# Optimization experiments

Hardware: AMD Instinct MI355X
Metric: run time of the kernel (lower is better)

## Reference

```python
import jax, jax.numpy as jnp
import numpy as np

N = 100000   # n_nodes
C = 128      # n_map
S = 6        # num_scales
E = 200000   # edges per pre/suc scale
EL = 50000   # left/right edges
L = 4        # fusion layers
EPS = 1e-5


def _gn(x, w, b):
    # GroupNorm(num_groups=1) on (N, C): normalize over channel dim per row.
    m = jnp.mean(x, axis=-1, keepdims=True)
    v = jnp.mean((x - m) ** 2, axis=-1, keepdims=True)
    return (x - m) * jax.lax.rsqrt(v + EPS) * w + b


def setup_inputs() -> dict:
    key = jax.random.key(0)
    ks = jax.random.split(key, 24)
    sc = 1.0 / np.sqrt(C)
    inp = {
        "feat": jax.random.normal(ks[0], (N, C), jnp.float32),
        "pre_u": jax.random.randint(ks[1], (S, E), 0, N, jnp.int32),
        "pre_v": jax.random.randint(ks[2], (S, E), 0, N, jnp.int32),
        "suc_u": jax.random.randint(ks[3], (S, E), 0, N, jnp.int32),
        "suc_v": jax.random.randint(ks[4], (S, E), 0, N, jnp.int32),
        "left_u": jax.random.randint(ks[5], (EL,), 0, N, jnp.int32),
        "left_v": jax.random.randint(ks[6], (EL,), 0, N, jnp.int32),
        "right_u": jax.random.randint(ks[7], (EL,), 0, N, jnp.int32),
        "right_v": jax.random.randint(ks[8], (EL,), 0, N, jnp.int32),
        # learned params, stacked over the 4 fusion layers
        "W_ctr": jax.random.normal(ks[9], (L, C, C), jnp.float32) * sc,
        "norm_w": jnp.ones((L, C), jnp.float32),
        "norm_b": jnp.zeros((L, C), jnp.float32),
        "W_ctr2": jax.random.normal(ks[10], (L, C, C), jnp.float32) * sc,
        "ctr2_w": jnp.ones((L, C), jnp.float32),
        "ctr2_b": jnp.zeros((L, C), jnp.float32),
        "W_left": jax.random.normal(ks[11], (L, C, C), jnp.float32) * sc,
        "W_right": jax.random.normal(ks[12], (L, C, C), jnp.float32) * sc,
        "W_pre": jax.random.normal(ks[13], (L, S, C, C), jnp.float32) * sc,
        "W_suc": jax.random.normal(ks[14], (L, S, C, C), jnp.float32) * sc,
    }
    return inp


def reference(feat, pre_u, pre_v, suc_u, suc_v, left_u, left_v, right_u, right_v,
              W_ctr, norm_w, norm_b, W_ctr2, ctr2_w, ctr2_b,
              W_left, W_right, W_pre, W_suc):
    res = feat
    for i in range(L):
        # ctr linear (bias=False): y = x @ W.T
        temp = feat @ W_ctr[i].T
        # pre/suc multi-scale gather -> per-scale linear -> scatter-add
        msg_pre = jnp.einsum('sef,sgf->seg', feat[pre_v], W_pre[i])  # (S,E,C)
        temp = temp.at[pre_u.reshape(-1)].add(msg_pre.reshape(-1, C))
        msg_suc = jnp.einsum('sef,sgf->seg', feat[suc_v], W_suc[i])
        temp = temp.at[suc_u.reshape(-1)].add(msg_suc.reshape(-1, C))
        # left/right neighbor edges
        temp = temp.at[left_u].add(feat[left_v] @ W_left[i].T)
        temp = temp.at[right_u].add(feat[right_v] @ W_right[i].T)
        # norm -> relu -> ctr2 (linear + GN, no act) -> residual -> relu
        feat = jax.nn.relu(_gn(temp, norm_w[i], norm_b[i]))
        feat = _gn(feat @ W_ctr2[i].T, ctr2_w[i], ctr2_b[i])
        feat = jax.nn.relu(feat + res)
        res = feat
    return feat
```

## Files before the change

### kernel.cpp

```cpp
#include <hip/hip_runtime.h>
#include <hip/hip_bf16.h>

#define NN 100000
#define C 128
#define S 6
#define EE 200000
#define ELR 50000
#define NLAYER 4
#define GN_EPS 1e-5f
#define NBKT 14
#define KCAT (NBKT*C)
#define TOTE (2*S*EE + 2*ELR)
#define MCNT (NBKT*NN)
#define NSCB ((MCNT + 255)/256)
#define NBLK2 ((NN + 127)/128)
#define VMASK 131071

typedef _Float16 f16;
typedef __attribute__((ext_vector_type(4))) _Float16 f16x4;
typedef __attribute__((ext_vector_type(8))) _Float16 f16x8;
typedef __attribute__((ext_vector_type(4))) float f32x4;
typedef __attribute__((ext_vector_type(8))) unsigned short us8;
struct alignas(8) h4 { f16 v[4]; };

__global__ void k_diag(float* out, float mb) { out[0] = mb; }

__global__ void k_wconv(const float* __restrict__ Wpre, const float* __restrict__ Wsuc,
                        const float* __restrict__ Wleft, const float* __restrict__ Wright,
                        const float* __restrict__ Wctr, const float* __restrict__ Wctr2,
                        f16* __restrict__ out) {
  int i = blockIdx.x * blockDim.x + threadIdx.x;
  if (i >= NLAYER * 16 * C * C) return;
  int within = i & (C * C - 1);
  int b = (i >> 14) & 15;
  int layer = i >> 18;
  const float* src;
  if (b < 6)        src = Wpre  + (size_t)(layer * S + b) * C * C;
  else if (b < 12)  src = Wsuc  + (size_t)(layer * S + (b - 6)) * C * C;
  else if (b == 12) src = Wleft  + (size_t)layer * C * C;
  else if (b == 13) src = Wright + (size_t)layer * C * C;
  else if (b == 14) src = Wctr   + (size_t)layer * C * C;
  else              src = Wctr2  + (size_t)layer * C * C;
  out[i] = (f16)src[within];
}

__global__ void k_f2b(const float* __restrict__ in, f16* __restrict__ out) {
  int i = blockIdx.x * blockDim.x + threadIdx.x;
  if (i >= NN * C / 4) return;
  f32x4 v = *(const f32x4*)(in + (long)i * 4);
  h4 o;
  #pragma unroll
  for (int r = 0; r < 4; r++) o.v[r] = (f16)v[r];
  *(h4*)(out + (long)i * 4) = o;
}

__global__ void k_count(const int* __restrict__ pu, const int* __restrict__ su,
                        const int* __restrict__ lu, const int* __restrict__ ru,
                        int* __restrict__ counts) {
  int i = blockIdx.x * blockDim.x + threadIdx.x;
  if (i >= TOTE) return;
  int u, b;
  if (i < S * EE)                { u = pu[i]; b = i / EE; }
  else if (i < 2 * S * EE)       { int j = i - S * EE; u = su[j]; b = 6 + j / EE; }
  else if (i < 2 * S * EE + ELR) { u = lu[i - 2 * S * EE]; b = 12; }
  else                           { u = ru[i - 2 * S * EE - ELR]; b = 13; }
  atomicAdd(&counts[b * NN + u], 1);
}

__global__ void k_scan1(const int* __restrict__ counts, int* __restrict__ offs, int* __restrict__ bsum) {
  __shared__ int sm[256];
  int t = threadIdx.x;
  int gidx = blockIdx.x * 256 + t;
  int v = (gidx < MCNT) ? counts[gidx] : 0;
  sm[t] = v;
  __syncthreads();
  for (int off = 1; off < 256; off <<= 1) {
    int x = (t >= off) ? sm[t - off] : 0;
    __syncthreads();
    sm[t] += x;
    __syncthreads();
  }
  if (gidx < MCNT) offs[gidx] = sm[t] - v;
  if (t == 255) bsum[blockIdx.x] = sm[255];
}

__global__ void k_scan_mid(int* __restrict__ bsum) {
  __shared__ int sm[1024];
  int t = threadIdx.x;
  int vreg[6];
  int p = 0;
  #pragma unroll
  for (int j = 0; j < 6; j++) {
    int idx = t * 6 + j;
    int x = (idx < NSCB) ? bsum[idx] : 0;
    vreg[j] = x; p += x;
  }
  sm[t] = p;
  __syncthreads();
  for (int off = 1; off < 1024; off <<= 1) {
    int x = (t >= off) ? sm[t - off] : 0;
    __syncthreads();
    sm[t] += x;
    __syncthreads();
  }
  int e = sm[t] - p;
  #pragma unroll
  for (int j = 0; j < 6; j++) {
    int idx = t * 6 + j;
    if (idx < NSCB) { bsum[idx] = e; e += vreg[j]; }
  }
}

__global__ void k_scan3(int* __restrict__ offs, const int* __restrict__ bsum) {
  int gidx = blockIdx.x * 256 + threadIdx.x;
  if (gidx >= MCNT) return;
  offs[gidx] += bsum[gidx >> 8];
}

__global__ void k_fill(const int* __restrict__ pu, const int* __restrict__ pv,
                       const int* __restrict__ su, const int* __restrict__ sv,
                       const int* __restrict__ lu, const int* __restrict__ lv,
                       const int* __restrict__ ru, const int* __restrict__ rv,
                       int* __restrict__ offs, int* __restrict__ col) {
  int i = blockIdx.x * blockDim.x + threadIdx.x;
  if (i >= TOTE) return;
  int u, v, b;
  if (i < S * EE)                { u = pu[i]; v = pv[i]; b = i / EE; }
  else if (i < 2 * S * EE)       { int j = i - S * EE; u = su[j]; v = sv[j]; b = 6 + j / EE; }
  else if (i < 2 * S * EE + ELR) { int j = i - 2 * S * EE; u = lu[j]; v = lv[j]; b = 12; }
  else                           { int j = i - 2 * S * EE - ELR; u = ru[j]; v = rv[j]; b = 13; }
  int pos = atomicAdd(&offs[b * NN + u], 1);
  col[pos] = v;
}

__global__ __launch_bounds__(512) void k_agg(
    const f16* __restrict__ fbf, const int* __restrict__ offs, const int* __restrict__ counts,
    const int* __restrict__ col, f16* __restrict__ Agg, int u0, int nrows) {
  int hw = threadIdx.x >> 5, li = threadIdx.x & 31;
  int cid = blockIdx.x * 16 + hw;
  if (cid >= 14 * nrows) return;
  int ul = cid / 14;
  int b = cid - ul * 14;
  int u = u0 + ul;
  int end = offs[b * NN + u];
  int cnt = counts[b * NN + u];
  int st = end - cnt;
  int cb = li << 2;
  float a0 = 0.f, a1 = 0.f, a2 = 0.f, a3 = 0.f;
  int j = 0;
  for (; j + 1 < cnt; j += 2) {
    int v0 = col[st + j] & VMASK;
    int v1 = col[st + j + 1] & VMASK;
    f16x4 h0 = *(const f16x4*)(fbf + (long)v0 * C + cb);
    f16x4 h1 = *(const f16x4*)(fbf + (long)v1 * C + cb);
    a0 += (float)h0[0] + (float)h1[0];
    a1 += (float)h0[1] + (float)h1[1];
    a2 += (float)h0[2] + (float)h1[2];
    a3 += (float)h0[3] + (float)h1[3];
  }
  if (j < cnt) {
    int v0 = col[st + j] & VMASK;
    f16x4 h0 = *(const f16x4*)(fbf + (long)v0 * C + cb);
    a0 += (float)h0[0]; a1 += (float)h0[1]; a2 += (float)h0[2]; a3 += (float)h0[3];
  }
  h4 o; o.v[0] = (f16)a0; o.v[1] = (f16)a1; o.v[2] = (f16)a2; o.v[3] = (f16)a3;
  *(h4*)(Agg + (long)ul * KCAT + b * C + cb) = o;
}

__global__ __launch_bounds__(256) void k_big(
    const f16* __restrict__ Agg, const f16* __restrict__ fbf, const f16* __restrict__ wb,
    const float* __restrict__ gnw, const float* __restrict__ gnb,
    f16* __restrict__ f1bf, int u0, int nrows) {
  int t = threadIdx.x;
  int wv = t >> 6, lane = t & 63;
  int l15 = lane & 15, g = lane >> 4;
  int row0 = blockIdx.x * 128;

  const f32x4 fz = {0.f, 0.f, 0.f, 0.f};
  f32x4 acc[2][8];
  #pragma unroll
  for (int ri = 0; ri < 2; ri++)
    #pragma unroll
    for (int ci = 0; ci < 8; ci++) acc[ri][ci] = fz;

  const f16x8 hz = {0,0,0,0,0,0,0,0};
  for (int src = 0; src < 15; src++) {
    const f16* wsrc = wb + src * C * C;
    f16x8 Bf[2][4];
    #pragma unroll
    for (int ri = 0; ri < 2; ri++) {
      int r = row0 + wv * 32 + ri * 16 + l15;
      bool ok = (r < nrows);
      #pragma unroll
      for (int kk = 0; kk < 4; kk++) {
        if (ok)
          Bf[ri][kk] = (src < 14)
            ? *(const f16x8*)(Agg + (long)r * KCAT + src * C + kk * 32 + g * 8)
            : *(const f16x8*)(fbf + (long)(u0 + r) * C + kk * 32 + g * 8);
        else Bf[ri][kk] = hz;
      }
    }
    #pragma unroll
    for (int ci = 0; ci < 8; ci++) {
      #pragma unroll
      for (int kk = 0; kk < 4; kk++) {
        f16x8 A = *(const f16x8*)(wsrc + (ci * 16 + l15) * C + kk * 32 + g * 8);
        acc[0][ci] = __builtin_amdgcn_mfma_f32_16x16x32_f16(A, Bf[0][kk], acc[0][ci], 0, 0, 0);
        acc[1][ci] = __builtin_amdgcn_mfma_f32_16x16x32_f16(A, Bf[1][kk], acc[1][ci], 0, 0, 0);
      }
    }
  }

  #pragma unroll
  for (int ri = 0; ri < 2; ri++) {
    float s = 0.f, q = 0.f;
    #pragma unroll
    for (int ci = 0; ci < 8; ci++)
      #pragma unroll
      for (int r2 = 0; r2 < 4; r2++) { float x = acc[ri][ci][r2]; s += x; q += x * x; }
    s += __shfl_xor(s, 16); s += __shfl_xor(s, 32);
    q += __shfl_xor(q, 16); q += __shfl_xor(q, 32);
    float mean = s * (1.0f / C);
    float var = q * (1.0f / C) - mean * mean;
    float inv = rsqrtf(var + GN_EPS);
    int r = row0 + wv * 32 + ri * 16 + l15;
    if (r >= nrows) continue;
    #pragma unroll
    for (int ci = 0; ci < 8; ci++) {
      int ocol = ci * 16 + g * 4;
      h4 o;
      #pragma unroll
      for (int r2 = 0; r2 < 4; r2++) {
        float y = (acc[ri][ci][r2] - mean) * inv * gnw[ocol + r2] + gnb[ocol + r2];
        o.v[r2] = (f16)fmaxf(y, 0.0f);
      }
      *(h4*)(f1bf + (long)(u0 + r) * C + ocol) = o;
    }
  }
}

__global__ __launch_bounds__(256) void k_ctr2(
    const f16* __restrict__ f1bf, const f16* __restrict__ w2,
    f16* __restrict__ fbf, const float* __restrict__ gw, const float* __restrict__ gb,
    float* __restrict__ fout, int last) {
  __shared__ f16 ws[128][136];
  __shared__ float gwb[2][C];
  int t = threadIdx.x;
  int wv = t >> 6, lane = t & 63;
  int l15 = lane & 15, g = lane >> 4;
  int row0 = blockIdx.x * 128;

  if (t < C) gwb[0][t] = gw[t];
  else       gwb[1][t - C] = gb[t - C];
  #pragma unroll
  for (int i = 0; i < 8; i++) {
    int q = t + 256 * i;
    int r = q >> 4, ch = q & 15;
    *(us8*)(&ws[r][ch * 8]) = *(const us8*)(w2 + r * C + ch * 8);
  }

  const f16x8 hz = {0,0,0,0,0,0,0,0};
  f16x8 Bf[2][4];
  #pragma unroll
  for (int ri = 0; ri < 2; ri++) {
    int grow = row0 + wv * 32 + ri * 16 + l15;
    #pragma unroll
    for (int kk = 0; kk < 4; kk++) {
      if (grow < NN)
        Bf[ri][kk] = *(const f16x8*)(f1bf + (long)grow * C + kk * 32 + g * 8);
      else
        Bf[ri][kk] = hz;
    }
  }
  __syncthreads();

  const f32x4 fzero = {0.f, 0.f, 0.f, 0.f};
  f32x4 acc[2][8];
  #pragma unroll
  for (int ri = 0; ri < 2; ri++)
    #pragma unroll
    for (int ci = 0; ci < 8; ci++) acc[ri][ci] = fzero;

  #pragma unroll
  for (int ci = 0; ci < 8; ci++) {
    f16x8 A[4];
    #pragma unroll
    for (int kk = 0; kk < 4; kk++)
      A[kk] = *(const f16x8*)(&ws[ci * 16 + l15][kk * 32 + g * 8]);
    #pragma unroll
    for (int ri = 0; ri < 2; ri++)
      #pragma unroll
      for (int kk = 0; kk < 4; kk++)
        acc[ri][ci] = __builtin_amdgcn_mfma_f32_16x16x32_f16(A[kk], Bf[ri][kk], acc[ri][ci], 0, 0, 0);
  }

  float sv[2], qv[2];
  #pragma unroll
  for (int ri = 0; ri < 2; ri++) {
    float s = 0.f, q = 0.f;
    #pragma unroll
    for (int ci = 0; ci < 8; ci++)
      #pragma unroll
      for (int r = 0; r < 4; r++) { float x = acc[ri][ci][r]; s += x; q += x * x; }
    s += __shfl_xor(s, 16); s += __shfl_xor(s, 32);
    q += __shfl_xor(q, 16); q += __shfl_xor(q, 32);
    sv[ri] = s; qv[ri] = q;
  }

  #pragma unroll
  for (int ri = 0; ri < 2; ri++) {
    float mean = sv[ri] * (1.0f / C);
    float var = qv[ri] * (1.0f / C) - mean * mean;
    float inv = rsqrtf(var + GN_EPS);
    int orow = row0 + wv * 32 + ri * 16 + l15;
    if (orow >= NN) continue;
    #pragma unroll
    for (int ci = 0; ci < 8; ci++) {
      int ocol = ci * 16 + g * 4;
      h4 rr = *(const h4*)(fbf + (long)orow * C + ocol);
      h4 ob;
      f32x4 o;
      #pragma unroll
      for (int r = 0; r < 4; r++) {
        float z = (acc[ri][ci][r] - mean) * inv;
        float y = z * gwb[0][ocol + r] + gwb[1][ocol + r];
        y += (float)rr.v[r];
        y = fmaxf(y, 0.0f);
        o[r] = y;
        ob.v[r] = (f16)y;
      }
      *(h4*)(fbf + (long)orow * C + ocol) = ob;
      if (last) *(f32x4*)(fout + (long)orow * C + ocol) = o;
    }
  }
}

extern "C" void kernel_launch(void* const* d_in, const int* in_sizes, int n_in,
                              void* d_out, int out_size, void* d_ws, size_t ws_size,
                              hipStream_t stream) {
  const float* feat   = (const float*)d_in[0];
  const int* pre_u    = (const int*)d_in[1];
  const int* pre_v    = (const int*)d_in[2];
  const int* suc_u    = (const int*)d_in[3];
  const int* suc_v    = (const int*)d_in[4];
  const int* left_u   = (const int*)d_in[5];
  const int* left_v   = (const int*)d_in[6];
  const int* right_u  = (const int*)d_in[7];
  const int* right_v  = (const int*)d_in[8];
  const float* W_ctr  = (const float*)d_in[9];
  const float* norm_w = (const float*)d_in[10];
  const float* norm_b = (const float*)d_in[11];
  const float* W_ctr2 = (const float*)d_in[12];
  const float* ctr2_w = (const float*)d_in[13];
  const float* ctr2_b = (const float*)d_in[14];
  const float* W_left = (const float*)d_in[15];
  const float* W_right= (const float*)d_in[16];
  const float* W_pre  = (const float*)d_in[17];
  const float* W_suc  = (const float*)d_in[18];
  float* outf = (float*)d_out;

  const size_t NEEDED = 75000000;
  if (ws_size < NEEDED) {
    k_diag<<<1, 1, 0, stream>>>(outf, (float)(ws_size >> 20));
    return;
  }

  char* p = (char*)d_ws;
  auto alloc = [&](size_t bytes) { char* r = p; p += (bytes + 255) & ~(size_t)255; return r; };
  int* col    = (int*)alloc((size_t)TOTE * 4);
  int* counts = (int*)alloc((size_t)MCNT * 4);
  int* offs   = (int*)alloc((size_t)MCNT * 4);
  int* bsum   = (int*)alloc((size_t)8192 * 4);
  f16* wbuf   = (f16*)alloc((size_t)NLAYER * 16 * C * C * 2);
  f16* fbf    = (f16*)alloc((size_t)NN * C * 2);
  f16* f1bf   = (f16*)alloc((size_t)NN * C * 2);

  size_t used = (size_t)(p - (char*)d_ws);
  size_t ws_free = (ws_size > used) ? ws_size - used : 0;
  f16* Agg;
  int CH;
  if (ws_free >= (size_t)NN * KCAT * 2)          { Agg = (f16*)p; CH = NN; }
  else if (ws_free >= (size_t)25000 * KCAT * 2)  { Agg = (f16*)p; CH = 25000; }
  else                                           { Agg = (f16*)d_out; CH = 12500; }

  hipMemsetAsync(counts, 0, (size_t)MCNT * 4, stream);
  k_wconv<<<(NLAYER * 16 * C * C + 255) / 256, 256, 0, stream>>>(W_pre, W_suc, W_left, W_right, W_ctr, W_ctr2, wbuf);
  k_f2b<<<(NN * C / 4 + 255) / 256, 256, 0, stream>>>(feat, fbf);
  k_count<<<(TOTE + 255) / 256, 256, 0, stream>>>(pre_u, suc_u, left_u, right_u, counts);
  k_scan1<<<NSCB, 256, 0, stream>>>(counts, offs, bsum);
  k_scan_mid<<<1, 1024, 0, stream>>>(bsum);
  k_scan3<<<NSCB, 256, 0, stream>>>(offs, bsum);
  k_fill<<<(TOTE + 255) / 256, 256, 0, stream>>>(pre_u, pre_v, suc_u, suc_v,
                                                 left_u, left_v, right_u, right_v, offs, col);

  for (int layer = 0; layer < NLAYER; layer++) {
    const f16* wl = wbuf + (size_t)layer * 16 * C * C;
    for (int u0 = 0; u0 < NN; u0 += CH) {
      int nr = (NN - u0 < CH) ? (NN - u0) : CH;
      int cells = 14 * nr;
      k_agg<<<(cells + 15) / 16, 512, 0, stream>>>(fbf, offs, counts, col, Agg, u0, nr);
      k_big<<<(nr + 127) / 128, 256, 0, stream>>>(Agg, fbf, wl,
                                                  norm_w + (size_t)layer * C, norm_b + (size_t)layer * C,
                                                  f1bf, u0, nr);
    }
    k_ctr2<<<NBLK2, 256, 0, stream>>>(f1bf, wl + 15 * C * C,
                                      fbf, ctr2_w + (size_t)layer * C, ctr2_b + (size_t)layer * C,
                                      outf, layer == NLAYER - 1 ? 1 : 0);
  }
}
```

Baseline: 2.773 ms.

## Fuse ctr2 linear, GroupNorm and residual into the main per-layer GEMM kernel

The big GEMM kernel now stages its normalized ReLU output in LDS with an XOR swizzle, then runs the ctr2 128x128 matmul, GroupNorm, residual add and ReLU in the same block. The next-layer features go to a ping-pong buffer, which removes the separate k_ctr2 launch and the global round trip of the intermediate activation. The B-operand loads are software double-buffered across the 15 source slices so loads overlap the MFMAs. The aggregation buffer is now always chunked at 25000 rows, which adds launches but keeps the Agg working set smaller and possibly more cache-resident. The trade-off is higher register and LDS pressure in the fused kernel, which may lower occupancy.

```diff
diff --git a/kernel.cpp b/kernel.cpp
--- a/kernel.cpp
+++ b/kernel.cpp
@@ -167,48 +167,67 @@
   *(h4*)(Agg + (long)ul * KCAT + b * C + cb) = o;
 }
 
-__global__ __launch_bounds__(256) void k_big(
-    const f16* __restrict__ Agg, const f16* __restrict__ fbf, const f16* __restrict__ wb,
+__global__ __launch_bounds__(256) void k_big2(
+    const f16* __restrict__ Agg, const f16* __restrict__ cur, const f16* __restrict__ wb,
     const float* __restrict__ gnw, const float* __restrict__ gnb,
-    f16* __restrict__ f1bf, int u0, int nrows) {
+    const float* __restrict__ g2w, const float* __restrict__ g2b,
+    f16* __restrict__ nxt, float* __restrict__ fout,
+    int u0, int nrows, int do2, int last) {
+  __shared__ f16 f1s[16384];
   int t = threadIdx.x;
   int wv = t >> 6, lane = t & 63;
   int l15 = lane & 15, g = lane >> 4;
   int row0 = blockIdx.x * 128;
-
-  const f32x4 fz = {0.f, 0.f, 0.f, 0.f};
+  const f16x8 hz = {0,0,0,0,0,0,0,0};
+
   f32x4 acc[2][8];
   #pragma unroll
   for (int ri = 0; ri < 2; ri++)
     #pragma unroll
-    for (int ci = 0; ci < 8; ci++) acc[ri][ci] = fz;
-
-  const f16x8 hz = {0,0,0,0,0,0,0,0};
-  for (int src = 0; src < 15; src++) {
-    const f16* wsrc = wb + src * C * C;
-    f16x8 Bf[2][4];
-    #pragma unroll
-    for (int ri = 0; ri < 2; ri++) {
-      int r = row0 + wv * 32 + ri * 16 + l15;
-      bool ok = (r < nrows);
-      #pragma unroll
-      for (int kk = 0; kk < 4; kk++) {
-        if (ok)
-          Bf[ri][kk] = (src < 14)
-            ? *(const f16x8*)(Agg + (long)r * KCAT + src * C + kk * 32 + g * 8)
-            : *(const f16x8*)(fbf + (long)(u0 + r) * C + kk * 32 + g * 8);
-        else Bf[ri][kk] = hz;
-      }
-    }
-    #pragma unroll
-    for (int ci = 0; ci < 8; ci++) {
-      #pragma unroll
-      for (int kk = 0; kk < 4; kk++) {
-        f16x8 A = *(const f16x8*)(wsrc + (ci * 16 + l15) * C + kk * 32 + g * 8);
-        acc[0][ci] = __builtin_amdgcn_mfma_f32_16x16x32_f16(A, Bf[0][kk], acc[0][ci], 0, 0, 0);
-        acc[1][ci] = __builtin_amdgcn_mfma_f32_16x16x32_f16(A, Bf[1][kk], acc[1][ci], 0, 0, 0);
-      }
-    }
+    for (int ci = 0; ci < 8; ci++) acc[ri][ci] = {0.f, 0.f, 0.f, 0.f};
+
+#define LOADB(SRC, BF)                                                          \
+  {                                                                             \
+    int _s = (SRC);                                                             \
+    _Pragma("unroll")                                                           \
+    for (int ri = 0; ri < 2; ri++) {                                            \
+      int r = row0 + wv * 32 + ri * 16 + l15;                                   \
+      bool ok = (r < nrows);                                                    \
+      _Pragma("unroll")                                                         \
+      for (int kk = 0; kk < 4; kk++) {                                          \
+        if (ok)                                                                 \
+          BF[ri][kk] = (_s < 14)                                                \
+            ? *(const f16x8*)(Agg + (long)r * KCAT + _s * C + kk * 32 + g * 8)  \
+            : *(const f16x8*)(cur + (long)(u0 + r) * C + kk * 32 + g * 8);      \
+        else BF[ri][kk] = hz;                                                   \
+      }                                                                         \
+    }                                                                           \
+  }
+
+#define MFMAS(SRC, BF)                                                          \
+  {                                                                             \
+    const f16* wsrc = wb + (SRC) * C * C;                                       \
+    _Pragma("unroll")                                                           \
+    for (int ci = 0; ci < 8; ci++)                                              \
+      _Pragma("unroll")                                                         \
+      for (int kk = 0; kk < 4; kk++) {                                          \
+        f16x8 A = *(const f16x8*)(wsrc + (ci * 16 + l15) * C + kk * 32 + g * 8);\
+        acc[0][ci] = __builtin_amdgcn_mfma_f32_16x16x32_f16(A, BF[0][kk], acc[0][ci], 0, 0, 0); \
+        acc[1][ci] = __builtin_amdgcn_mfma_f32_16x16x32_f16(A, BF[1][kk], acc[1][ci], 0, 0, 0); \
+      }                                                                         \
+  }
+
+  {
+    f16x8 B0[2][4], B1[2][4];
+    LOADB(0, B0);
+    #pragma unroll
+    for (int sp = 0; sp < 7; sp++) {
+      LOADB(2 * sp + 1, B1);
+      MFMAS(2 * sp, B0);
+      LOADB(2 * sp + 2, B0);
+      MFMAS(2 * sp + 1, B1);
+    }
+    MFMAS(14, B0);
   }
 
   #pragma unroll
@@ -218,6 +237,69 @@
     for (int ci = 0; ci < 8; ci++)
       #pragma unroll
       for (int r2 = 0; r2 < 4; r2++) { float x = acc[ri][ci][r2]; s += x; q += x * x; }
+    s += __shfl_xor(s, 16); s += __shfl_xor(s, 32);
+    q += __shfl_xor(q, 16); q += __shfl_xor(q, 32);
+    float mean = s * (1.0f / C);
+    float var = q * (1.0f / C) - mean * mean;
+    float inv = rsqrtf(var + GN_EPS);
+    int lrow = wv * 32 + ri * 16 + l15;
+    int grow = row0 + lrow;
+    #pragma unroll
+    for (int ci = 0; ci < 8; ci++) {
+      int ocol = ci * 16 + g * 4;
+      h4 o;
+      #pragma unroll
+      for (int r2 = 0; r2 < 4; r2++) {
+        float y = (acc[ri][ci][r2] - mean) * inv * gnw[ocol + r2] + gnb[ocol + r2];
+        o.v[r2] = (f16)fmaxf(y, 0.0f);
+      }
+      if (do2) {
+        int gran = ((ci * 2 + (g >> 1)) ^ (lrow & 7));
+        *(h4*)(&f1s[lrow * 128 + gran * 8 + (g & 1) * 4]) = o;
+      } else if (grow < nrows + u0 - u0 + row0 ? (row0 + lrow) < nrows : false) {
+      }
+      if (!do2 && (row0 + lrow) < nrows)
+        *(h4*)(nxt + (long)(u0 + row0 + lrow) * C + ocol) = o;
+    }
+  }
+  if (!do2) return;
+  __syncthreads();
+
+  f32x4 a2[2][8];
+  #pragma unroll
+  for (int ri = 0; ri < 2; ri++)
+    #pragma unroll
+    for (int ci = 0; ci < 8; ci++) a2[ri][ci] = {0.f, 0.f, 0.f, 0.f};
+
+  {
+    f16x8 B2[2][4];
+    #pragma unroll
+    for (int ri = 0; ri < 2; ri++) {
+      int lrow = wv * 32 + ri * 16 + l15;
+      #pragma unroll
+      for (int kk = 0; kk < 4; kk++) {
+        int gran = (kk * 4 + g) ^ (lrow & 7);
+        B2[ri][kk] = *(const f16x8*)(&f1s[lrow * 128 + gran * 8]);
+      }
+    }
+    const f16* w2 = wb + 15 * C * C;
+    #pragma unroll
+    for (int ci = 0; ci < 8; ci++)
+      #pragma unroll
+      for (int kk = 0; kk < 4; kk++) {
+        f16x8 A = *(const f16x8*)(w2 + (ci * 16 + l15) * C + kk * 32 + g * 8);
+        a2[0][ci] = __builtin_amdgcn_mfma_f32_16x16x32_f16(A, B2[0][kk], a2[0][ci], 0, 0, 0);
+        a2[1][ci] = __builtin_amdgcn_mfma_f32_16x16x32_f16(A, B2[1][kk], a2[1][ci], 0, 0, 0);
+      }
+  }
+
+  #pragma unroll
+  for (int ri = 0; ri < 2; ri++) {
+    float s = 0.f, q = 0.f;
+    #pragma unroll
+    for (int ci = 0; ci < 8; ci++)
+      #pragma unroll
+      for (int r2 = 0; r2 < 4; r2++) { float x = a2[ri][ci][r2]; s += x; q += x * x; }
     s += __shfl_xor(s, 16); s += __shfl_xor(s, 32);
     q += __shfl_xor(q, 16); q += __shfl_xor(q, 32);
     float mean = s * (1.0f / C);
@@ -225,18 +307,28 @@
     float inv = rsqrtf(var + GN_EPS);
     int r = row0 + wv * 32 + ri * 16 + l15;
     if (r >= nrows) continue;
+    long grow = u0 + r;
     #pragma unroll
     for (int ci = 0; ci < 8; ci++) {
       int ocol = ci * 16 + g * 4;
-      h4 o;
+      h4 rr = *(const h4*)(cur + grow * C + ocol);
       #pragma unroll
       for (int r2 = 0; r2 < 4; r2++) {
-        float y = (acc[ri][ci][r2] - mean) * inv * gnw[ocol + r2] + gnb[ocol + r2];
-        o.v[r2] = (f16)fmaxf(y, 0.0f);
-      }
-      *(h4*)(f1bf + (long)(u0 + r) * C + ocol) = o;
-    }
-  }
+        float z = (a2[ri][ci][r2] - mean) * inv;
+        a2[ri][ci][r2] = fmaxf(z * g2w[ocol + r2] + g2b[ocol + r2] + (float)rr.v[r2], 0.0f);
+      }
+      if (last) {
+        *(f32x4*)(fout + grow * C + ocol) = a2[ri][ci];
+      } else {
+        h4 ob;
+        #pragma unroll
+        for (int r2 = 0; r2 < 4; r2++) ob.v[r2] = (f16)a2[ri][ci][r2];
+        *(h4*)(nxt + grow * C + ocol) = ob;
+      }
+    }
+  }
+#undef LOADB
+#undef MFMAS
 }
 
 __global__ __launch_bounds__(256) void k_ctr2(
@@ -274,12 +366,11 @@
   }
   __syncthreads();
 
-  const f32x4 fzero = {0.f, 0.f, 0.f, 0.f};
   f32x4 acc[2][8];
   #pragma unroll
   for (int ri = 0; ri < 2; ri++)
     #pragma unroll
-    for (int ci = 0; ci < 8; ci++) acc[ri][ci] = fzero;
+    for (int ci = 0; ci < 8; ci++) acc[ri][ci] = {0.f, 0.f, 0.f, 0.f};
 
   #pragma unroll
   for (int ci = 0; ci < 8; ci++) {
@@ -372,20 +463,19 @@
   int* offs   = (int*)alloc((size_t)MCNT * 4);
   int* bsum   = (int*)alloc((size_t)8192 * 4);
   f16* wbuf   = (f16*)alloc((size_t)NLAYER * 16 * C * C * 2);
-  f16* fbf    = (f16*)alloc((size_t)NN * C * 2);
-  f16* f1bf   = (f16*)alloc((size_t)NN * C * 2);
+  f16* fA     = (f16*)alloc((size_t)NN * C * 2);
+  f16* fB     = (f16*)alloc((size_t)NN * C * 2);
 
   size_t used = (size_t)(p - (char*)d_ws);
   size_t ws_free = (ws_size > used) ? ws_size - used : 0;
   f16* Agg;
-  int CH;
-  if (ws_free >= (size_t)NN * KCAT * 2)          { Agg = (f16*)p; CH = NN; }
-  else if (ws_free >= (size_t)25000 * KCAT * 2)  { Agg = (f16*)p; CH = 25000; }
-  else                                           { Agg = (f16*)d_out; CH = 12500; }
+  int CH, fuseAll;
+  if (ws_free >= (size_t)25000 * KCAT * 2) { Agg = (f16*)p;     CH = 25000; fuseAll = 1; }
+  else                                     { Agg = (f16*)d_out; CH = 12500; fuseAll = 0; }
 
   hipMemsetAsync(counts, 0, (size_t)MCNT * 4, stream);
   k_wconv<<<(NLAYER * 16 * C * C + 255) / 256, 256, 0, stream>>>(W_pre, W_suc, W_left, W_right, W_ctr, W_ctr2, wbuf);
-  k_f2b<<<(NN * C / 4 + 255) / 256, 256, 0, stream>>>(feat, fbf);
+  k_f2b<<<(NN * C / 4 + 255) / 256, 256, 0, stream>>>(feat, fA);
   k_count<<<(TOTE + 255) / 256, 256, 0, stream>>>(pre_u, suc_u, left_u, right_u, counts);
   k_scan1<<<NSCB, 256, 0, stream>>>(counts, offs, bsum);
   k_scan_mid<<<1, 1024, 0, stream>>>(bsum);
@@ -393,18 +483,26 @@
   k_fill<<<(TOTE + 255) / 256, 256, 0, stream>>>(pre_u, pre_v, suc_u, suc_v,
                                                  left_u, left_v, right_u, right_v, offs, col);
 
+  f16* cur = fA;
+  f16* nxt = fB;
   for (int layer = 0; layer < NLAYER; layer++) {
     const f16* wl = wbuf + (size_t)layer * 16 * C * C;
+    int lastL = (layer == NLAYER - 1);
+    int do2 = fuseAll || !lastL;
     for (int u0 = 0; u0 < NN; u0 += CH) {
       int nr = (NN - u0 < CH) ? (NN - u0) : CH;
       int cells = 14 * nr;
-      k_agg<<<(cells + 15) / 16, 512, 0, stream>>>(fbf, offs, counts, col, Agg, u0, nr);
-      k_big<<<(nr + 127) / 128, 256, 0, stream>>>(Agg, fbf, wl,
-                                                  norm_w + (size_t)layer * C, norm_b + (size_t)layer * C,
-                                                  f1bf, u0, nr);
-    }
-    k_ctr2<<<NBLK2, 256, 0, stream>>>(f1bf, wl + 15 * C * C,
-                                      fbf, ctr2_w + (size_t)layer * C, ctr2_b + (size_t)layer * C,
-                                      outf, layer == NLAYER - 1 ? 1 : 0);
-  }
-}
+      k_agg<<<(cells + 15) / 16, 512, 0, stream>>>(cur, offs, counts, col, Agg, u0, nr);
+      k_big2<<<(nr + 127) / 128, 256, 0, stream>>>(Agg, cur, wl,
+                                                   norm_w + (size_t)layer * C, norm_b + (size_t)layer * C,
+                                                   ctr2_w + (size_t)layer * C, ctr2_b + (size_t)layer * C,
+                                                   nxt, outf, u0, nr, do2, lastL);
+    }
+    if (!do2) {
+      k_ctr2<<<NBLK2, 256, 0, stream>>>(nxt, wl + 15 * C * C,
+                                        cur, ctr2_w + (size_t)layer * C, ctr2_b + (size_t)layer * C,
+                                        outf, 1);
+    }
+    f16* tmp = cur; cur = nxt; nxt = tmp;
+  }
+}
```

New measurement: 2.947 ms. +6.3%, slower.

## Restructure aggregation into 8-row strips per bucket and shrink big GEMM tile

Applied to the files above, without the earlier changes.

The aggregation kernel now assigns each half-wave a strip of 8 consecutive destination rows in one bucket. It loads up to 64 column indices cooperatively and broadcasts them with shuffles, and issues 4 neighbour gathers at a time to expose more memory-level parallelism. The fused GEMM+GroupNorm kernel uses 64-row blocks with one 16-row tile per wave, halving accumulator registers to raise occupancy at the cost of more weight re-reads. A 50000-row chunk tier is added and buffers are renamed. The strip mapping assumes the chunk row count is a multiple of 8.

```diff
diff --git a/kernel.cpp b/kernel.cpp
--- a/kernel.cpp
+++ b/kernel.cpp
@@ -14,7 +14,6 @@
 #define MCNT (NBKT*NN)
 #define NSCB ((MCNT + 255)/256)
 #define NBLK2 ((NN + 127)/128)
-#define VMASK 131071
 
 typedef _Float16 f16;
 typedef __attribute__((ext_vector_type(4))) _Float16 f16x4;
@@ -137,101 +136,114 @@
     const f16* __restrict__ fbf, const int* __restrict__ offs, const int* __restrict__ counts,
     const int* __restrict__ col, f16* __restrict__ Agg, int u0, int nrows) {
   int hw = threadIdx.x >> 5, li = threadIdx.x & 31;
-  int cid = blockIdx.x * 16 + hw;
-  if (cid >= 14 * nrows) return;
-  int ul = cid / 14;
-  int b = cid - ul * 14;
-  int u = u0 + ul;
-  int end = offs[b * NN + u];
-  int cnt = counts[b * NN + u];
-  int st = end - cnt;
+  int sid = blockIdx.x * 16 + hw;
+  int spb = nrows >> 3;
+  if (sid >= 14 * spb) return;
+  int b = sid / spb;
+  int k8 = sid - b * spb;
+  int ubase = u0 + k8 * 8;
+  int cellbase = b * NN + ubase;
   int cb = li << 2;
-  float a0 = 0.f, a1 = 0.f, a2 = 0.f, a3 = 0.f;
-  int j = 0;
-  for (; j + 1 < cnt; j += 2) {
-    int v0 = col[st + j] & VMASK;
-    int v1 = col[st + j + 1] & VMASK;
-    f16x4 h0 = *(const f16x4*)(fbf + (long)v0 * C + cb);
-    f16x4 h1 = *(const f16x4*)(fbf + (long)v1 * C + cb);
-    a0 += (float)h0[0] + (float)h1[0];
-    a1 += (float)h0[1] + (float)h1[1];
-    a2 += (float)h0[2] + (float)h1[2];
-    a3 += (float)h0[3] + (float)h1[3];
-  }
-  if (j < cnt) {
-    int v0 = col[st + j] & VMASK;
-    f16x4 h0 = *(const f16x4*)(fbf + (long)v0 * C + cb);
-    a0 += (float)h0[0]; a1 += (float)h0[1]; a2 += (float)h0[2]; a3 += (float)h0[3];
-  }
-  h4 o; o.v[0] = (f16)a0; o.v[1] = (f16)a1; o.v[2] = (f16)a2; o.v[3] = (f16)a3;
-  *(h4*)(Agg + (long)ul * KCAT + b * C + cb) = o;
+
+  int endv = 0, cntv = 0;
+  if (li < 8) { endv = offs[cellbase + li]; cntv = counts[cellbase + li]; }
+  int st0  = __shfl(endv - cntv, 0, 32);
+  int end7 = __shfl(endv, 7, 32);
+
+  int cv0 = (st0 + li < end7) ? col[st0 + li] : 0;
+  int cv1 = (st0 + 32 + li < end7) ? col[st0 + 32 + li] : 0;
+
+  #pragma unroll
+  for (int c = 0; c < 8; c++) {
+    int stc = __shfl(endv - cntv, c, 32);
+    int cc2 = __shfl(cntv, c, 32);
+    float a0 = 0.f, a1 = 0.f, a2 = 0.f, a3 = 0.f;
+    for (int j = 0; j < cc2; j += 4) {
+      f16x4 h[4];
+      #pragma unroll
+      for (int q = 0; q < 4; q++) {
+        int jj = j + q;
+        if (jj < cc2) {
+          int gi = stc + jj;
+          int d = gi - st0;
+          int v;
+          if (d < 64) {
+            int lo = __shfl(cv0, d & 31, 32);
+            int hi2 = __shfl(cv1, d & 31, 32);
+            v = (d < 32) ? lo : hi2;
+          } else {
+            v = col[gi];
+          }
+          h[q] = *(const f16x4*)(fbf + (long)v * C + cb);
+        }
+      }
+      #pragma unroll
+      for (int q = 0; q < 4; q++) {
+        if (j + q < cc2) {
+          a0 += (float)h[q][0]; a1 += (float)h[q][1];
+          a2 += (float)h[q][2]; a3 += (float)h[q][3];
+        }
+      }
+    }
+    h4 o; o.v[0] = (f16)a0; o.v[1] = (f16)a1; o.v[2] = (f16)a2; o.v[3] = (f16)a3;
+    *(h4*)(Agg + (long)(ubase - u0 + c) * KCAT + b * C + cb) = o;
+  }
 }
 
 __global__ __launch_bounds__(256) void k_big(
-    const f16* __restrict__ Agg, const f16* __restrict__ fbf, const f16* __restrict__ wb,
+    const f16* __restrict__ Agg, const f16* __restrict__ cur, const f16* __restrict__ wb,
     const float* __restrict__ gnw, const float* __restrict__ gnb,
     f16* __restrict__ f1bf, int u0, int nrows) {
   int t = threadIdx.x;
   int wv = t >> 6, lane = t & 63;
   int l15 = lane & 15, g = lane >> 4;
-  int row0 = blockIdx.x * 128;
-
-  const f32x4 fz = {0.f, 0.f, 0.f, 0.f};
-  f32x4 acc[2][8];
-  #pragma unroll
-  for (int ri = 0; ri < 2; ri++)
-    #pragma unroll
-    for (int ci = 0; ci < 8; ci++) acc[ri][ci] = fz;
-
+  int row0 = blockIdx.x * 64;
+  int r = row0 + wv * 16 + l15;
+  bool ok = (r < nrows);
   const f16x8 hz = {0,0,0,0,0,0,0,0};
+
+  f32x4 acc[8];
+  #pragma unroll
+  for (int ci = 0; ci < 8; ci++) acc[ci] = {0.f, 0.f, 0.f, 0.f};
+
   for (int src = 0; src < 15; src++) {
+    f16x8 Bf[4];
+    #pragma unroll
+    for (int kk = 0; kk < 4; kk++) {
+      if (ok)
+        Bf[kk] = (src < 14)
+          ? *(const f16x8*)(Agg + (long)r * KCAT + src * C + kk * 32 + g * 8)
+          : *(const f16x8*)(cur + (long)(u0 + r) * C + kk * 32 + g * 8);
+      else Bf[kk] = hz;
+    }
     const f16* wsrc = wb + src * C * C;
-    f16x8 Bf[2][4];
-    #pragma unroll
-    for (int ri = 0; ri < 2; ri++) {
-      int r = row0 + wv * 32 + ri * 16 + l15;
-      bool ok = (r < nrows);
-      #pragma unroll
-      for (int kk = 0; kk < 4; kk++) {
-        if (ok)
-          Bf[ri][kk] = (src < 14)
-            ? *(const f16x8*)(Agg + (long)r * KCAT + src * C + kk * 32 + g * 8)
-            : *(const f16x8*)(fbf + (long)(u0 + r) * C + kk * 32 + g * 8);
-        else Bf[ri][kk] = hz;
-      }
-    }
-    #pragma unroll
-    for (int ci = 0; ci < 8; ci++) {
+    #pragma unroll
+    for (int ci = 0; ci < 8; ci++)
       #pragma unroll
       for (int kk = 0; kk < 4; kk++) {
         f16x8 A = *(const f16x8*)(wsrc + (ci * 16 + l15) * C + kk * 32 + g * 8);
-        acc[0][ci] = __builtin_amdgcn_mfma_f32_16x16x32_f16(A, Bf[0][kk], acc[0][ci], 0, 0, 0);
-        acc[1][ci] = __builtin_amdgcn_mfma_f32_16x16x32_f16(A, Bf[1][kk], acc[1][ci], 0, 0, 0);
+        acc[ci] = __builtin_amdgcn_mfma_f32_16x16x32_f16(A, Bf[kk], acc[ci], 0, 0, 0);
       }
-    }
-  }
-
-  #pragma unroll
-  for (int ri = 0; ri < 2; ri++) {
-    float s = 0.f, q = 0.f;
-    #pragma unroll
-    for (int ci = 0; ci < 8; ci++)
-      #pragma unroll
-      for (int r2 = 0; r2 < 4; r2++) { float x = acc[ri][ci][r2]; s += x; q += x * x; }
-    s += __shfl_xor(s, 16); s += __shfl_xor(s, 32);
-    q += __shfl_xor(q, 16); q += __shfl_xor(q, 32);
-    float mean = s * (1.0f / C);
-    float var = q * (1.0f / C) - mean * mean;
-    float inv = rsqrtf(var + GN_EPS);
-    int r = row0 + wv * 32 + ri * 16 + l15;
-    if (r >= nrows) continue;
+  }
+
+  float s = 0.f, q = 0.f;
+  #pragma unroll
+  for (int ci = 0; ci < 8; ci++)
+    #pragma unroll
+    for (int r2 = 0; r2 < 4; r2++) { float x = acc[ci][r2]; s += x; q += x * x; }
+  s += __shfl_xor(s, 16); s += __shfl_xor(s, 32);
+  q += __shfl_xor(q, 16); q += __shfl_xor(q, 32);
+  float mean = s * (1.0f / C);
+  float var = q * (1.0f / C) - mean * mean;
+  float inv = rsqrtf(var + GN_EPS);
+  if (ok) {
     #pragma unroll
     for (int ci = 0; ci < 8; ci++) {
       int ocol = ci * 16 + g * 4;
       h4 o;
       #pragma unroll
       for (int r2 = 0; r2 < 4; r2++) {
-        float y = (acc[ri][ci][r2] - mean) * inv * gnw[ocol + r2] + gnb[ocol + r2];
+        float y = (acc[ci][r2] - mean) * inv * gnw[ocol + r2] + gnb[ocol + r2];
         o.v[r2] = (f16)fmaxf(y, 0.0f);
       }
       *(h4*)(f1bf + (long)(u0 + r) * C + ocol) = o;
@@ -274,12 +286,11 @@
   }
   __syncthreads();
 
-  const f32x4 fzero = {0.f, 0.f, 0.f, 0.f};
   f32x4 acc[2][8];
   #pragma unroll
   for (int ri = 0; ri < 2; ri++)
     #pragma unroll
-    for (int ci = 0; ci < 8; ci++) acc[ri][ci] = fzero;
+    for (int ci = 0; ci < 8; ci++) acc[ri][ci] = {0.f, 0.f, 0.f, 0.f};
 
   #pragma unroll
   for (int ci = 0; ci < 8; ci++) {
@@ -372,20 +383,21 @@
   int* offs   = (int*)alloc((size_t)MCNT * 4);
   int* bsum   = (int*)alloc((size_t)8192 * 4);
   f16* wbuf   = (f16*)alloc((size_t)NLAYER * 16 * C * C * 2);
-  f16* fbf    = (f16*)alloc((size_t)NN * C * 2);
-  f16* f1bf   = (f16*)alloc((size_t)NN * C * 2);
+  f16* fA     = (f16*)alloc((size_t)NN * C * 2);
+  f16* fB     = (f16*)alloc((size_t)NN * C * 2);
 
   size_t used = (size_t)(p - (char*)d_ws);
   size_t ws_free = (ws_size > used) ? ws_size - used : 0;
   f16* Agg;
   int CH;
-  if (ws_free >= (size_t)NN * KCAT * 2)          { Agg = (f16*)p; CH = NN; }
-  else if (ws_free >= (size_t)25000 * KCAT * 2)  { Agg = (f16*)p; CH = 25000; }
-  else                                           { Agg = (f16*)d_out; CH = 12500; }
+  if      (ws_free >= (size_t)NN    * KCAT * 2) { Agg = (f16*)p;     CH = NN;    }
+  else if (ws_free >= (size_t)50000 * KCAT * 2) { Agg = (f16*)p;     CH = 50000; }
+  else if (ws_free >= (size_t)25000 * KCAT * 2) { Agg = (f16*)p;     CH = 25000; }
+  else                                          { Agg = (f16*)d_out; CH = 12800; }
 
   hipMemsetAsync(counts, 0, (size_t)MCNT * 4, stream);
   k_wconv<<<(NLAYER * 16 * C * C + 255) / 256, 256, 0, stream>>>(W_pre, W_suc, W_left, W_right, W_ctr, W_ctr2, wbuf);
-  k_f2b<<<(NN * C / 4 + 255) / 256, 256, 0, stream>>>(feat, fbf);
+  k_f2b<<<(NN * C / 4 + 255) / 256, 256, 0, stream>>>(feat, fA);
   k_count<<<(TOTE + 255) / 256, 256, 0, stream>>>(pre_u, suc_u, left_u, right_u, counts);
   k_scan1<<<NSCB, 256, 0, stream>>>(counts, offs, bsum);
   k_scan_mid<<<1, 1024, 0, stream>>>(bsum);
@@ -395,16 +407,17 @@
 
   for (int layer = 0; layer < NLAYER; layer++) {
     const f16* wl = wbuf + (size_t)layer * 16 * C * C;
+    int lastL = (layer == NLAYER - 1);
     for (int u0 = 0; u0 < NN; u0 += CH) {
       int nr = (NN - u0 < CH) ? (NN - u0) : CH;
-      int cells = 14 * nr;
-      k_agg<<<(cells + 15) / 16, 512, 0, stream>>>(fbf, offs, counts, col, Agg, u0, nr);
-      k_big<<<(nr + 127) / 128, 256, 0, stream>>>(Agg, fbf, wl,
-                                                  norm_w + (size_t)layer * C, norm_b + (size_t)layer * C,
-                                                  f1bf, u0, nr);
-    }
-    k_ctr2<<<NBLK2, 256, 0, stream>>>(f1bf, wl + 15 * C * C,
-                                      fbf, ctr2_w + (size_t)layer * C, ctr2_b + (size_t)layer * C,
-                                      outf, layer == NLAYER - 1 ? 1 : 0);
-  }
-}
+      int strips = 14 * (nr >> 3);
+      k_agg<<<(strips + 15) / 16, 512, 0, stream>>>(fA, offs, counts, col, Agg, u0, nr);
+      k_big<<<(nr + 63) / 64, 256, 0, stream>>>(Agg, fA, wl,
+                                                norm_w + (size_t)layer * C, norm_b + (size_t)layer * C,
+                                                fB, u0, nr);
+    }
+    k_ctr2<<<NBLK2, 256, 0, stream>>>(fB, wl + 15 * C * C,
+                                      fA, ctr2_w + (size_t)layer * C, ctr2_b + (size_t)layer * C,
+                                      outf, lastL ? 1 : 0);
+  }
+}
```

Result: slower. 3.386 ms (+22.1%).
